# Kernel optimization log

Hardware: AMD Instinct MI355X
Metric: run time of the kernel (lower is better)

Reference implementation:

```python
import jax, jax.numpy as jnp
import numpy as np

EPS = 1e-7  # K.epsilon()
NUM_ROUTING = 3

def squash(s, axis=-1):
    sq = jnp.sum(jnp.square(s), axis=axis, keepdims=True)
    scale = sq / (1.0 + sq) / jnp.sqrt(sq + EPS)
    return scale * s

def setup_inputs() -> dict:
    key = jax.random.key(0)
    k1, k2 = jax.random.split(key)
    B, INC, IND = 512, 1152, 8   # batch, input_num_capsule, input_dim_capsule
    NC, DC = 10, 16              # num_capsule, dim_capsule
    inputs = jax.random.normal(k1, (B, INC, IND), dtype=jnp.float32)
    W = jax.random.normal(k2, (NC, INC, DC, IND), dtype=jnp.float32) * 0.05
    return {"inputs": inputs, "W": W}

def reference(inputs, W):
    # u_hat[b,j,i,d] = sum_k inputs[b,i,k] * W[j,i,d,k]
    u_hat = jnp.einsum('bik,jidk->bjid', inputs, W)  # [B, NC, INC, DC]
    b = jnp.zeros(u_hat.shape[:3], dtype=u_hat.dtype)  # [B, NC, INC]
    v = None
    for i in range(NUM_ROUTING):
        c = jax.nn.softmax(b, axis=1)                  # softmax over output capsules
        s = jnp.einsum('bji,bjid->bjd', c, u_hat)      # weighted sum over input caps
        v = squash(s)                                  # [B, NC, DC]
        if i < NUM_ROUTING - 1:
            b = b + jnp.einsum('bjd,bjid->bji', v, u_hat)  # agreement update
    return v
```

## Files before the change

### kernel.cpp

```cpp
#include <hip/hip_runtime.h>


#define NB 512
#define NI 1152
#define NJ 10
#define ND 16

typedef short          bf16x8 __attribute__((ext_vector_type(8)));
typedef unsigned short u16x8  __attribute__((ext_vector_type(8)));
typedef float          f32x4  __attribute__((ext_vector_type(4)));

constexpr float EPS_ = 1e-7f;

constexpr size_t XB_ELEMS = (size_t)NB * NI * 8;
constexpr size_t WB_ELEMS = (size_t)NJ * NI * ND * 8;
constexpr int    XQ = 1179648;
constexpr int    WQ = 368640;
constexpr int    NIGB = 144;

__device__ inline unsigned short f2bf(float f) {
    unsigned u = __float_as_uint(f);
    return (unsigned short)((u + 0x7fffu + ((u >> 16) & 1u)) >> 16);
}
__device__ inline float bf2f(unsigned short u) {
    return __uint_as_float((unsigned)u << 16);
}

__global__ __launch_bounds__(256)
void conv_bf16(const float* __restrict__ x, const float* __restrict__ Wg,
               unsigned short* __restrict__ xb, unsigned short* __restrict__ wb)
{
    int t = blockIdx.x * 256 + threadIdx.x;
    if (t < XQ) {
        float4 v = ((const float4*)x)[t];
        ushort4 o; o.x=f2bf(v.x); o.y=f2bf(v.y); o.z=f2bf(v.z); o.w=f2bf(v.w);
        ((ushort4*)xb)[t] = o;
    } else if (t - XQ < WQ) {
        int u = t - XQ;
        float4 v = ((const float4*)Wg)[u];
        ushort4 o; o.x=f2bf(v.x); o.y=f2bf(v.y); o.z=f2bf(v.z); o.w=f2bf(v.w);
        ((ushort4*)wb)[u] = o;
    }
}

template <int MODE>
__global__ __launch_bounds__(256, 2)
void caps_pass(const unsigned short* __restrict__ xb,
               const unsigned short* __restrict__ wb,
               const float* __restrict__ vsum_g,
               unsigned short* __restrict__ part)
{
    __shared__ __align__(16) char smem[28688];
    unsigned short* wl = (unsigned short*)smem;
    unsigned short* xl = (unsigned short*)(smem + 20480);
    unsigned short* zp = (unsigned short*)(smem + 28672);

    const int tid = threadIdx.x, lane = tid & 63, w = tid >> 6;
    const int bl = lane & 15, kg = lane >> 4;
    const int bg = blockIdx.x, ig = blockIdx.y;
    const int i0 = ig * 8, b0 = bg * 64;
    const int b  = b0 + w * 16 + bl;
    const int brow = w * 16 + bl;

    if (tid < 8) zp[tid] = 0;

#pragma unroll
    for (int r = 0; r < 5; ++r) {
        int g  = tid + r * 256;
        int il = g / 160, rem = g - il * 160;
        const unsigned short* src =
            wb + ((size_t)(rem >> 4) * NI + (i0 + il)) * 128 + (rem & 15) * 8;
        *(u16x8*)(wl + g * 8) = *(const u16x8*)src;
    }
#pragma unroll
    for (int r = 0; r < 2; ++r) {
        int g  = tid + r * 256;
        int br = g >> 3, sg = g & 7;
        int gr = sg ^ (br & 7);
        *(u16x8*)(xl + g * 8) =
            *(const u16x8*)(xb + ((size_t)(b0 + br) * NI + i0 + gr) * 8);
    }

    f32x4 vs[NJ];
    if (MODE == 1) {
#pragma unroll
        for (int j = 0; j < NJ; ++j)
            vs[j] = *(const f32x4*)(vsum_g + (size_t)b * 160 + j * 16 + kg * 4);
    }

    __syncthreads();

    const f32x4 zero = {0.f, 0.f, 0.f, 0.f};
    f32x4 sacc[NJ];
#pragma unroll
    for (int j = 0; j < NJ; ++j) sacc[j] = zero;

#pragma unroll 2
    for (int it = 0; it < 8; ++it) {
        bf16x8 xv = *(const bf16x8*)(xl + (brow * 8 + (it ^ (brow & 7))) * 8);

        f32x4 uh[NJ];
#pragma unroll
        for (int j = 0; j < NJ; ++j) {
            const unsigned short* ap = (kg == 0)
                ? (wl + ((it * 10 + j) * 16 + bl) * 8) : zp;
            bf16x8 af = *(const bf16x8*)ap;
            if (MODE == 0)
                sacc[j] = __builtin_amdgcn_mfma_f32_16x16x32_bf16(af, xv, sacc[j], 0, 0, 0);
            else
                uh[j] = __builtin_amdgcn_mfma_f32_16x16x32_bf16(af, xv, zero, 0, 0, 0);
        }

        if (MODE == 1) {
            float bd[NJ];
#pragma unroll
            for (int j = 0; j < NJ; ++j) {
                float v = uh[j][0] * vs[j][0] + uh[j][1] * vs[j][1]
                        + uh[j][2] * vs[j][2] + uh[j][3] * vs[j][3];
                v += __shfl_xor(v, 16, 64);
                v += __shfl_xor(v, 32, 64);
                bd[j] = v;
            }
            float m01 = fmaxf(bd[0], bd[1]), m23 = fmaxf(bd[2], bd[3]);
            float m45 = fmaxf(bd[4], bd[5]), m67 = fmaxf(bd[6], bd[7]);
            float m89 = fmaxf(bd[8], bd[9]);
            float m = fmaxf(fmaxf(fmaxf(m01, m23), fmaxf(m45, m67)), m89);
#pragma unroll
            for (int j = 0; j < NJ; ++j) bd[j] = __expf(bd[j] - m);
            float Z = ((bd[0] + bd[1]) + (bd[2] + bd[3]))
                    + ((bd[4] + bd[5]) + (bd[6] + bd[7])) + (bd[8] + bd[9]);
            const float rZ = 1.f / Z;
#pragma unroll
            for (int j = 0; j < NJ; ++j) {
                const float c = bd[j] * rZ;
                sacc[j] += c * uh[j];
            }
        }
    }

    __syncthreads();
    unsigned short* s16 = (unsigned short*)smem;
#pragma unroll
    for (int j = 0; j < NJ; ++j) {
        ushort4 o;
        o.x = f2bf(sacc[j][0]); o.y = f2bf(sacc[j][1]);
        o.z = f2bf(sacc[j][2]); o.w = f2bf(sacc[j][3]);
        *(ushort4*)(s16 + brow * 168 + j * 16 + kg * 4) = o;
    }
    __syncthreads();
    unsigned short* pp = part + ((size_t)ig * NB + b0) * 160;
#pragma unroll
    for (int r = 0; r < 5; ++r) {
        int idx = tid + r * 256;
        int row = idx / 20, ch = idx - row * 20;
        *(u16x8*)(pp + idx * 8) = *(const u16x8*)(s16 + row * 168 + ch * 8);
    }
}

__global__ __launch_bounds__(256)
void squash_reduce(const unsigned short* __restrict__ part,
                   float* __restrict__ vsum_g, float* __restrict__ out,
                   float alpha, int mode)
{
    const int t = blockIdx.x * 256 + threadIdx.x;
    const unsigned short* p = part + t;
    float a0 = 0.f, a1 = 0.f, a2 = 0.f, a3 = 0.f;
#pragma unroll 4
    for (int ig = 0; ig < NIGB; ig += 4) {
        a0 += bf2f(p[(size_t)ig * 81920]);
        a1 += bf2f(p[(size_t)(ig + 1) * 81920]);
        a2 += bf2f(p[(size_t)(ig + 2) * 81920]);
        a3 += bf2f(p[(size_t)(ig + 3) * 81920]);
    }
    const float s = ((a0 + a1) + (a2 + a3)) * alpha;

    float sq = s * s;
    sq += __shfl_xor(sq, 1, 64);
    sq += __shfl_xor(sq, 2, 64);
    sq += __shfl_xor(sq, 4, 64);
    sq += __shfl_xor(sq, 8, 64);
    const float sc = sq / ((1.f + sq) * sqrtf(sq + EPS_));
    const float v  = sc * s;

    if (mode == 0)      vsum_g[t] = v;
    else if (mode == 1) vsum_g[t] += v;
    else                out[t] = v;
}

extern "C" void kernel_launch(void* const* d_in, const int* in_sizes, int n_in,
                              void* d_out, int out_size, void* d_ws, size_t ws_size,
                              hipStream_t stream)
{
    const float* inp = (const float*)d_in[0];
    const float* Wg  = (const float*)d_in[1];
    float* out = (float*)d_out;

    unsigned short* xbp  = (unsigned short*)d_ws;
    unsigned short* wbp  = xbp + XB_ELEMS;
    unsigned short* part = wbp + WB_ELEMS;
    float* vsum = (float*)(part + (size_t)NIGB * NB * 160);

    conv_bf16<<<(XQ + WQ + 255) / 256, 256, 0, stream>>>(inp, Wg, xbp, wbp);

    dim3 grid(8, NIGB);
    caps_pass<0><<<grid, 256, 0, stream>>>(xbp, wbp, nullptr, part);
    squash_reduce<<<320, 256, 0, stream>>>(part, vsum, out, 0.1f, 0);
    caps_pass<1><<<grid, 256, 0, stream>>>(xbp, wbp, vsum, part);
    squash_reduce<<<320, 256, 0, stream>>>(part, vsum, out, 1.0f, 1);
    caps_pass<1><<<grid, 256, 0, stream>>>(xbp, wbp, vsum, part);
    squash_reduce<<<320, 256, 0, stream>>>(part, vsum, out, 1.0f, 2);
}
```

Before: 166.7 us.

## Pack four input capsules into each MFMA K dimension and pad LDS layout

Mode 0 now fills all four K-groups of the 16x16x32 MFMA with four different input capsules, so each instruction sums over four capsules instead of one plus zero padding. That cuts the MFMA count in that pass by four. Mode 1 loads full A fragments once per four capsules and masks the B operand per capsule, which keeps per-capsule u_hat for the softmax but does not reduce MFMA count. The W and x shared-memory layouts are padded (161 and 9 strides) in place of the XOR swizzle to avoid bank conflicts, and the zero-page buffer is removed.

New measurement: 163.8 us. Within noise of the previous version (-1.7%).

```diff
diff --git a/kernel.cpp b/kernel.cpp
--- a/kernel.cpp
+++ b/kernel.cpp
@@ -50,10 +50,9 @@
                const float* __restrict__ vsum_g,
                unsigned short* __restrict__ part)
 {
-    __shared__ __align__(16) char smem[28688];
+    __shared__ __align__(16) char smem[30368];
     unsigned short* wl = (unsigned short*)smem;
-    unsigned short* xl = (unsigned short*)(smem + 20480);
-    unsigned short* zp = (unsigned short*)(smem + 28672);
+    unsigned short* xl = (unsigned short*)(smem + 20608);
 
     const int tid = threadIdx.x, lane = tid & 63, w = tid >> 6;
     const int bl = lane & 15, kg = lane >> 4;
@@ -62,23 +61,22 @@
     const int b  = b0 + w * 16 + bl;
     const int brow = w * 16 + bl;
 
-    if (tid < 8) zp[tid] = 0;
-
 #pragma unroll
     for (int r = 0; r < 5; ++r) {
         int g  = tid + r * 256;
         int il = g / 160, rem = g - il * 160;
         const unsigned short* src =
             wb + ((size_t)(rem >> 4) * NI + (i0 + il)) * 128 + (rem & 15) * 8;
-        *(u16x8*)(wl + g * 8) = *(const u16x8*)src;
+        *(u16x8*)(wl + (il * 161 + rem) * 8) = *(const u16x8*)src;
     }
 #pragma unroll
     for (int r = 0; r < 2; ++r) {
-        int g  = tid + r * 256;
-        int br = g >> 3, sg = g & 7;
-        int gr = sg ^ (br & 7);
-        *(u16x8*)(xl + g * 8) =
-            *(const u16x8*)(xb + ((size_t)(b0 + br) * NI + i0 + gr) * 8);
+        int g = tid + r * 256;
+        if (g < 512) {
+            int br = g >> 3, il = g & 7;
+            *(u16x8*)(xl + (br * 9 + il) * 8) =
+                *(const u16x8*)(xb + ((size_t)(b0 + br) * NI + i0 + il) * 8);
+        }
     }
 
     f32x4 vs[NJ];
@@ -90,50 +88,57 @@
 
     __syncthreads();
 
-    const f32x4 zero = {0.f, 0.f, 0.f, 0.f};
+    const f32x4  zero  = {0.f, 0.f, 0.f, 0.f};
+    const bf16x8 zerob = {0, 0, 0, 0, 0, 0, 0, 0};
     f32x4 sacc[NJ];
 #pragma unroll
     for (int j = 0; j < NJ; ++j) sacc[j] = zero;
 
-#pragma unroll 2
-    for (int it = 0; it < 8; ++it) {
-        bf16x8 xv = *(const bf16x8*)(xl + (brow * 8 + (it ^ (brow & 7))) * 8);
-
-        f32x4 uh[NJ];
-#pragma unroll
-        for (int j = 0; j < NJ; ++j) {
-            const unsigned short* ap = (kg == 0)
-                ? (wl + ((it * 10 + j) * 16 + bl) * 8) : zp;
-            bf16x8 af = *(const bf16x8*)ap;
-            if (MODE == 0)
-                sacc[j] = __builtin_amdgcn_mfma_f32_16x16x32_bf16(af, xv, sacc[j], 0, 0, 0);
-            else
-                uh[j] = __builtin_amdgcn_mfma_f32_16x16x32_bf16(af, xv, zero, 0, 0, 0);
-        }
-
-        if (MODE == 1) {
-            float bd[NJ];
-#pragma unroll
-            for (int j = 0; j < NJ; ++j) {
-                float v = uh[j][0] * vs[j][0] + uh[j][1] * vs[j][1]
-                        + uh[j][2] * vs[j][2] + uh[j][3] * vs[j][3];
-                v += __shfl_xor(v, 16, 64);
-                v += __shfl_xor(v, 32, 64);
-                bd[j] = v;
-            }
-            float m01 = fmaxf(bd[0], bd[1]), m23 = fmaxf(bd[2], bd[3]);
-            float m45 = fmaxf(bd[4], bd[5]), m67 = fmaxf(bd[6], bd[7]);
-            float m89 = fmaxf(bd[8], bd[9]);
-            float m = fmaxf(fmaxf(fmaxf(m01, m23), fmaxf(m45, m67)), m89);
-#pragma unroll
-            for (int j = 0; j < NJ; ++j) bd[j] = __expf(bd[j] - m);
-            float Z = ((bd[0] + bd[1]) + (bd[2] + bd[3]))
-                    + ((bd[4] + bd[5]) + (bd[6] + bd[7])) + (bd[8] + bd[9]);
-            const float rZ = 1.f / Z;
-#pragma unroll
-            for (int j = 0; j < NJ; ++j) {
-                const float c = bd[j] * rZ;
-                sacc[j] += c * uh[j];
+#pragma unroll
+    for (int t4 = 0; t4 < 2; ++t4) {
+        bf16x8 afull[NJ];
+#pragma unroll
+        for (int j = 0; j < NJ; ++j)
+            afull[j] = *(const bf16x8*)(wl + (((t4 * 4 + kg) * 161) + j * 16 + bl) * 8);
+
+        if (MODE == 0) {
+            bf16x8 xv = *(const bf16x8*)(xl + (brow * 9 + t4 * 4 + kg) * 8);
+#pragma unroll
+            for (int j = 0; j < NJ; ++j)
+                sacc[j] = __builtin_amdgcn_mfma_f32_16x16x32_bf16(afull[j], xv, sacc[j], 0, 0, 0);
+        } else {
+            bf16x8 xv = *(const bf16x8*)(xl + (brow * 9 + t4 * 4 + kg) * 8);
+#pragma unroll
+            for (int q = 0; q < 4; ++q) {
+                const bf16x8 bq = (kg == q) ? xv : zerob;
+                f32x4 uh[NJ];
+#pragma unroll
+                for (int j = 0; j < NJ; ++j)
+                    uh[j] = __builtin_amdgcn_mfma_f32_16x16x32_bf16(afull[j], bq, zero, 0, 0, 0);
+
+                float bd[NJ];
+#pragma unroll
+                for (int j = 0; j < NJ; ++j) {
+                    float v = uh[j][0] * vs[j][0] + uh[j][1] * vs[j][1]
+                            + uh[j][2] * vs[j][2] + uh[j][3] * vs[j][3];
+                    v += __shfl_xor(v, 16, 64);
+                    v += __shfl_xor(v, 32, 64);
+                    bd[j] = v;
+                }
+                float m01 = fmaxf(bd[0], bd[1]), m23 = fmaxf(bd[2], bd[3]);
+                float m45 = fmaxf(bd[4], bd[5]), m67 = fmaxf(bd[6], bd[7]);
+                float m89 = fmaxf(bd[8], bd[9]);
+                float m = fmaxf(fmaxf(fmaxf(m01, m23), fmaxf(m45, m67)), m89);
+#pragma unroll
+                for (int j = 0; j < NJ; ++j) bd[j] = __expf(bd[j] - m);
+                float Z = ((bd[0] + bd[1]) + (bd[2] + bd[3]))
+                        + ((bd[4] + bd[5]) + (bd[6] + bd[7])) + (bd[8] + bd[9]);
+                const float rZ = 1.f / Z;
+#pragma unroll
+                for (int j = 0; j < NJ; ++j) {
+                    const float c = bd[j] * rZ;
+                    sacc[j] += c * uh[j];
+                }
             }
         }
     }
```
